# Optimization experiments

Hardware: AMD Instinct MI355X
Metric: run time of the kernel (lower is better)

The kernel has to match this reference:

```python
import jax, jax.numpy as jnp
import numpy as np

DS = 4  # pooling / upsample factor


def _avg_pool(t, ds):
    B, C, H, W = t.shape
    return t.reshape(B, C, H // ds, ds, W // ds, ds).mean(axis=(3, 5))


def setup_inputs() -> dict:
    key = jax.random.key(0)
    ks = jax.random.split(key, 8)
    B, C, H, W = 8, 512, 128, 128
    Ck = C // 4
    inp = jax.random.normal(ks[0], (B, C, H, W), dtype=jnp.float32)
    c2 = jax.random.normal(ks[1], (B, C, H, W), dtype=jnp.float32)
    # 1x1 conv weights == dense matrices over channel dim (with bias, as nn.Conv2d default)
    Wq = jax.random.normal(ks[2], (Ck, C), dtype=jnp.float32) * 0.02
    bq = jax.random.normal(ks[3], (Ck,), dtype=jnp.float32) * 0.02
    Wk = jax.random.normal(ks[4], (Ck, C), dtype=jnp.float32) * 0.02
    bk = jax.random.normal(ks[5], (Ck,), dtype=jnp.float32) * 0.02
    Wv = jax.random.normal(ks[6], (C, C), dtype=jnp.float32) * 0.02
    bv = jax.random.normal(ks[7], (C,), dtype=jnp.float32) * 0.02
    return {"input": inp, "c2": c2, "Wq": Wq, "bq": bq, "Wk": Wk, "bk": bk, "Wv": Wv, "bv": bv}


def reference(input, c2, Wq, bq, Wk, bk, Wv, bv):
    # Note: the torch module's `gamma` parameter is NOT used in forward; faithful omission.
    x = _avg_pool(input, DS)  # [B,C,h,w]
    y = _avg_pool(c2, DS)
    B, C, h, w = x.shape
    N = h * w
    Ck = Wq.shape[0]
    xf = x.reshape(B, C, N)
    yf = y.reshape(B, C, N)
    q = jnp.einsum('oc,bcn->bon', Wq, xf) + bq[None, :, None]  # [B,Ck,N]
    k = jnp.einsum('oc,bcn->bon', Wk, yf) + bk[None, :, None]  # [B,Ck,N]
    v = jnp.einsum('oc,bcn->bon', Wv, yf) + bv[None, :, None]  # [B,C,N]
    scale = jnp.asarray(Ck, x.dtype) ** -0.5
    energy = jnp.einsum('bon,bom->bnm', q, k) * scale  # [B,N,N] = q^T k
    attn = jax.nn.softmax(energy, axis=-1)
    out = jnp.einsum('bcm,bnm->bcn', v, attn)  # v @ attn^T
    out = out.reshape(B, C, h, w)
    # F.interpolate with default mode='nearest' and size = exact integer multiple -> repeat
    out = jnp.repeat(jnp.repeat(out, DS, axis=2), DS, axis=3)
    return out + c2
```

## Files before the change

### kernel.cpp

```cpp
#include <hip/hip_runtime.h>
#include <stdint.h>
#include <stddef.h>

#define Bn   8
#define Cn   512
#define CKn  128
#define Hn   128
#define Nn   1024

typedef float f32x4 __attribute__((ext_vector_type(4)));
typedef short bf16x8 __attribute__((ext_vector_type(8)));

__device__ __forceinline__ uint16_t f2b(float f) {
  uint32_t x = __float_as_uint(f);
  uint32_t r = (x + 0x7FFFu + ((x >> 16) & 1u)) >> 16;
  return (uint16_t)r;
}

__device__ __forceinline__ void gld_lds16(const uint16_t* g, short* lds_base, int lane) {
#if __has_builtin(__builtin_amdgcn_global_load_lds)
  __builtin_amdgcn_global_load_lds(
      (const __attribute__((address_space(1))) void*)g,
      (__attribute__((address_space(3))) void*)lds_base, 16, 0, 0);
#else
  *(bf16x8*)(lds_base + lane * 8) = *(const bf16x8*)g;
#endif
}

__device__ __forceinline__ void gemm128(const uint16_t* __restrict__ A,
                                        const uint16_t* __restrict__ Bt,
                                        int lda, int ldb, int K,
                                        short* As, short* Bs, f32x4 acc[4][4]) {
  const int tid  = threadIdx.x;
  const int lane = tid & 63;
  const int wave = tid >> 6;
  const int quad = lane >> 4, l16 = lane & 15;
  const int rin  = lane >> 2, cc = lane & 3;
  const int wr = wave >> 1, wc = wave & 1;
  for (int kt = 0; kt < K; kt += 32) {
    __syncthreads();
    gld_lds16(A  + (size_t)(wave * 32 +      rin) * lda + kt + cc * 8, As + wave * 1024,       lane);
    gld_lds16(A  + (size_t)(wave * 32 + 16 + rin) * lda + kt + cc * 8, As + wave * 1024 + 512, lane);
    gld_lds16(Bt + (size_t)(wave * 32 +      rin) * ldb + kt + cc * 8, Bs + wave * 1024,       lane);
    gld_lds16(Bt + (size_t)(wave * 32 + 16 + rin) * ldb + kt + cc * 8, Bs + wave * 1024 + 512, lane);
    __syncthreads();
    bf16x8 af[4], bfr[4];
#pragma unroll
    for (int i = 0; i < 4; ++i)
      af[i] = *(const bf16x8*)(As + (wr * 64 + i * 16 + l16) * 32 + quad * 8);
#pragma unroll
    for (int j = 0; j < 4; ++j)
      bfr[j] = *(const bf16x8*)(Bs + (wc * 64 + j * 16 + l16) * 32 + quad * 8);
#pragma unroll
    for (int i = 0; i < 4; ++i)
#pragma unroll
      for (int j = 0; j < 4; ++j)
        acc[i][j] = __builtin_amdgcn_mfma_f32_16x16x32_bf16(af[i], bfr[j], acc[i][j], 0, 0, 0);
  }
}

#define EPI_VARS \
  const int lane = threadIdx.x & 63; const int wave = threadIdx.x >> 6; \
  const int quad = lane >> 4, l16 = lane & 15; \
  const int wr = wave >> 1, wc = wave & 1;

__global__ __launch_bounds__(256) void wconv_kernel(
    const float* __restrict__ Wq, const float* __restrict__ Wk, const float* __restrict__ Wv,
    uint16_t* __restrict__ Wqb, uint16_t* __restrict__ Wkb, uint16_t* __restrict__ Wvb) {
  int i = blockIdx.x * 256 + threadIdx.x;
  if (i < CKn * Cn) { Wqb[i] = f2b(Wq[i]); Wkb[i] = f2b(Wk[i]); }
  Wvb[i] = f2b(Wv[i]);
}

__global__ __launch_bounds__(1024) void pool_kernel(
    const float* __restrict__ input, const float* __restrict__ c2,
    uint16_t* __restrict__ xT, uint16_t* __restrict__ yT) {
  const int cblk = blockIdx.x, ph = blockIdx.y;
  const int b = blockIdx.z >> 1, src = blockIdx.z & 1;
  const float* in = src ? c2 : input;
  uint16_t* out = src ? yT : xT;
  const int tw = threadIdx.x & 31, tc = threadIdx.x >> 5;
  const int c = cblk * 32 + tc;
  const float* p = in + (((size_t)(b * Cn + c) * Hn) + ph * 4) * Hn + tw * 4;
  float s = 0.f;
#pragma unroll
  for (int r = 0; r < 4; ++r) {
    float4 t = *(const float4*)(p + (size_t)r * Hn);
    s += t.x + t.y + t.z + t.w;
  }
  __shared__ float tile[32][33];
  tile[tw][tc] = s * 0.0625f;
  __syncthreads();
  const int tn = threadIdx.x >> 5, tcc = threadIdx.x & 31;
  out[((size_t)b * Nn + ph * 32 + tn) * Cn + cblk * 32 + tcc] = f2b(tile[tn][tcc]);
}

__global__ __launch_bounds__(256) void qkv_kernel(
    const uint16_t* __restrict__ Wqb, const uint16_t* __restrict__ Wkb, const uint16_t* __restrict__ Wvb,
    const float* __restrict__ bq, const float* __restrict__ bk, const float* __restrict__ bv,
    const uint16_t* __restrict__ xT, const uint16_t* __restrict__ yT,
    uint16_t* __restrict__ qT, uint16_t* __restrict__ kT, uint16_t* __restrict__ vm) {
  __shared__ short As[4096], Bs[4096];
  const int b = blockIdx.y;
  const int r = blockIdx.x;
  const int mt = r >> 3, nt = r & 7;
  int op, m0; const uint16_t* A; const float* bias;
  if (mt == 0)      { op = 0; m0 = 0;              A = Wqb;                     bias = bq; }
  else if (mt == 1) { op = 1; m0 = 0;              A = Wkb;                     bias = bk; }
  else              { op = 2; m0 = (mt - 2) * 128; A = Wvb + (size_t)m0 * Cn;   bias = bv; }
  const uint16_t* Bt = ((op == 0) ? xT : yT) + (size_t)b * Nn * Cn + (size_t)nt * 128 * Cn;
  f32x4 acc[4][4];
#pragma unroll
  for (int i = 0; i < 4; ++i)
#pragma unroll
    for (int j = 0; j < 4; ++j) acc[i][j] = (f32x4)0.f;
  gemm128(A, Bt, Cn, Cn, Cn, As, Bs, acc);
  EPI_VARS;
#pragma unroll
  for (int i = 0; i < 4; ++i)
#pragma unroll
    for (int j = 0; j < 4; ++j)
#pragma unroll
      for (int rg = 0; rg < 4; ++rg) {
        int m = m0 + wr * 64 + i * 16 + quad * 4 + rg;
        int n = nt * 128 + wc * 64 + j * 16 + l16;
        float val = acc[i][j][rg] + bias[m];
        if (op == 2) vm[(size_t)(b * Cn + m) * Nn + n] = f2b(val);
        else {
          uint16_t* dst = (op == 0) ? qT : kT;
          dst[(size_t)(b * Nn + n) * CKn + m] = f2b(val);
        }
      }
}

__global__ __launch_bounds__(1024) void esm_kernel(
    const uint16_t* __restrict__ qT, const uint16_t* __restrict__ kT,
    uint16_t* __restrict__ attn) {
  const int b = blockIdx.y, n0 = blockIdx.x * 16;
  const int tid = threadIdx.x, lane = tid & 63, w = tid >> 6;
  const int quad = lane >> 4, l16 = lane & 15;
  const uint16_t* qb = qT + (size_t)(b * Nn + n0) * CKn;
  const uint16_t* kb = kT + (size_t)(b * Nn + w * 64) * CKn;
  f32x4 acc[4];
#pragma unroll
  for (int j = 0; j < 4; ++j) acc[j] = (f32x4)0.f;
#pragma unroll
  for (int kt = 0; kt < CKn; kt += 32) {
    bf16x8 af = *(const bf16x8*)(qb + (size_t)l16 * CKn + kt + quad * 8);
    bf16x8 bfr[4];
#pragma unroll
    for (int j = 0; j < 4; ++j)
      bfr[j] = *(const bf16x8*)(kb + (size_t)(j * 16 + l16) * CKn + kt + quad * 8);
#pragma unroll
    for (int j = 0; j < 4; ++j)
      acc[j] = __builtin_amdgcn_mfma_f32_16x16x32_bf16(af, bfr[j], acc[j], 0, 0, 0);
  }
  const float scale = 0.08838834764831845f;
#pragma unroll
  for (int j = 0; j < 4; ++j) acc[j] *= scale;

  __shared__ float red[16][16];
  __shared__ float gout[16];
  float mx[4];
#pragma unroll
  for (int rg = 0; rg < 4; ++rg) {
    mx[rg] = fmaxf(fmaxf(acc[0][rg], acc[1][rg]), fmaxf(acc[2][rg], acc[3][rg]));
#pragma unroll
    for (int off = 1; off < 16; off <<= 1) mx[rg] = fmaxf(mx[rg], __shfl_xor(mx[rg], off, 64));
  }
  if (l16 == 0) {
#pragma unroll
    for (int rg = 0; rg < 4; ++rg) red[quad * 4 + rg][w] = mx[rg];
  }
  __syncthreads();
  if (tid < 16) {
    float g = -3.4e38f;
#pragma unroll
    for (int ww = 0; ww < 16; ++ww) g = fmaxf(g, red[tid][ww]);
    gout[tid] = g;
  }
  __syncthreads();
  float rmax[4];
#pragma unroll
  for (int rg = 0; rg < 4; ++rg) rmax[rg] = gout[quad * 4 + rg];
  float sm[4] = {0.f, 0.f, 0.f, 0.f};
#pragma unroll
  for (int j = 0; j < 4; ++j)
#pragma unroll
    for (int rg = 0; rg < 4; ++rg) {
      float p = __expf(acc[j][rg] - rmax[rg]);
      acc[j][rg] = p;
      sm[rg] += p;
    }
#pragma unroll
  for (int rg = 0; rg < 4; ++rg)
#pragma unroll
    for (int off = 1; off < 16; off <<= 1) sm[rg] += __shfl_xor(sm[rg], off, 64);
  if (l16 == 0) {
#pragma unroll
    for (int rg = 0; rg < 4; ++rg) red[quad * 4 + rg][w] = sm[rg];
  }
  __syncthreads();
  if (tid < 16) {
    float s = 0.f;
#pragma unroll
    for (int ww = 0; ww < 16; ++ww) s += red[tid][ww];
    gout[tid] = 1.f / s;
  }
  __syncthreads();
#pragma unroll
  for (int rg = 0; rg < 4; ++rg) {
    float inv = gout[quad * 4 + rg];
    uint16_t* arow = attn + (size_t)(b * Nn + n0 + quad * 4 + rg) * Nn + w * 64;
#pragma unroll
    for (int j = 0; j < 4; ++j) arow[j * 16 + l16] = f2b(acc[j][rg] * inv);
  }
}

__global__ __launch_bounds__(256) void outup_kernel(
    const uint16_t* __restrict__ vm, const uint16_t* __restrict__ attn,
    const float* __restrict__ c2, float* __restrict__ out) {
  __shared__ short As[4096], Bs[4096];
  const int b = blockIdx.y;
  const int r = blockIdx.x, mt = r >> 3, nt = r & 7;
  const uint16_t* A  = vm   + (size_t)b * Cn * Nn + (size_t)mt * 128 * Nn;
  const uint16_t* Bt = attn + (size_t)b * Nn * Nn + (size_t)nt * 128 * Nn;
  f32x4 acc[4][4];
#pragma unroll
  for (int i = 0; i < 4; ++i)
#pragma unroll
    for (int j = 0; j < 4; ++j) acc[i][j] = (f32x4)0.f;
  gemm128(A, Bt, Nn, Nn, Nn, As, Bs, acc);
  EPI_VARS;
#pragma unroll
  for (int i = 0; i < 4; ++i)
#pragma unroll
    for (int j = 0; j < 4; ++j) {
      const int n  = nt * 128 + wc * 64 + j * 16 + l16;
      const int ph = n >> 5, pw = n & 31;
#pragma unroll
      for (int rg = 0; rg < 4; ++rg) {
        const int c = mt * 128 + wr * 64 + i * 16 + quad * 4 + rg;
        const float v = acc[i][j][rg];
        const size_t base = (((size_t)(b * Cn + c) * Hn) + ph * 4) * Hn + pw * 4;
#pragma unroll
        for (int rr = 0; rr < 4; ++rr) {
          float4 t4 = *(const float4*)(c2 + base + (size_t)rr * Hn);
          t4.x += v; t4.y += v; t4.z += v; t4.w += v;
          *(float4*)(out + base + (size_t)rr * Hn) = t4;
        }
      }
    }
}

extern "C" void kernel_launch(void* const* d_in, const int* in_sizes, int n_in,
                              void* d_out, int out_size, void* d_ws, size_t ws_size,
                              hipStream_t stream) {
  const float* input = (const float*)d_in[0];
  const float* c2    = (const float*)d_in[1];
  const float* Wq    = (const float*)d_in[2];
  const float* bq    = (const float*)d_in[3];
  const float* Wk    = (const float*)d_in[4];
  const float* bk    = (const float*)d_in[5];
  const float* Wv    = (const float*)d_in[6];
  const float* bv    = (const float*)d_in[7];
  float* out = (float*)d_out;
  uint8_t* ws = (uint8_t*)d_ws;

  uint16_t* xT   = (uint16_t*)(ws + 0);
  uint16_t* yT   = (uint16_t*)(ws + 8388608);
  uint16_t* Wqb  = (uint16_t*)(ws + 16777216);
  uint16_t* Wkb  = (uint16_t*)(ws + 16908288);
  uint16_t* Wvb  = (uint16_t*)(ws + 17039360);
  uint16_t* qT   = (uint16_t*)(ws + 17563648);
  uint16_t* kT   = (uint16_t*)(ws + 19660800);
  uint16_t* vm   = (uint16_t*)(ws + 21757952);
  uint16_t* attn = (uint16_t*)(ws + 30146560);

  hipLaunchKernelGGL(wconv_kernel, dim3(1024), dim3(256), 0, stream,
                     Wq, Wk, Wv, Wqb, Wkb, Wvb);
  hipLaunchKernelGGL(pool_kernel, dim3(16, 32, 16), dim3(1024), 0, stream,
                     input, c2, xT, yT);
  hipLaunchKernelGGL(qkv_kernel, dim3(48, 8), dim3(256), 0, stream,
                     Wqb, Wkb, Wvb, bq, bk, bv, xT, yT, qT, kT, vm);
  hipLaunchKernelGGL(esm_kernel, dim3(64, 8), dim3(1024), 0, stream, qT, kT, attn);
  hipLaunchKernelGGL(outup_kernel, dim3(32, 8), dim3(256), 0, stream,
                     vm, attn, c2, out);
}
```

Measured before the change: 722.9 us.

## Split output GEMM from upsample-add and use 64x128 tiles

```diff
diff --git a/kernel.cpp b/kernel.cpp
--- a/kernel.cpp
+++ b/kernel.cpp
@@ -59,6 +59,30 @@
   }
 }
 
+__device__ __forceinline__ void gemm64x128(const uint16_t* __restrict__ A,
+                                           const uint16_t* __restrict__ Bt,
+                                           int lda, int ldb, int K,
+                                           short* As, short* Bs, f32x4 acc[8]) {
+  const int tid  = threadIdx.x;
+  const int lane = tid & 63;
+  const int wave = tid >> 6;
+  const int quad = lane >> 4, l16 = lane & 15;
+  const int rin  = lane >> 2, cc = lane & 3;
+  for (int kt = 0; kt < K; kt += 32) {
+    __syncthreads();
+    gld_lds16(A + (size_t)(wave * 16 + rin) * lda + kt + cc * 8, As + wave * 512, lane);
+    gld_lds16(Bt + (size_t)(wave * 32 + rin) * ldb + kt + cc * 8, Bs + wave * 1024, lane);
+    gld_lds16(Bt + (size_t)(wave * 32 + 16 + rin) * ldb + kt + cc * 8, Bs + wave * 1024 + 512, lane);
+    __syncthreads();
+    bf16x8 af = *(const bf16x8*)(As + (wave * 16 + l16) * 32 + quad * 8);
+#pragma unroll
+    for (int j = 0; j < 8; ++j) {
+      bf16x8 bfr = *(const bf16x8*)(Bs + (j * 16 + l16) * 32 + quad * 8);
+      acc[j] = __builtin_amdgcn_mfma_f32_16x16x32_bf16(af, bfr, acc[j], 0, 0, 0);
+    }
+  }
+}
+
 #define EPI_VARS \
   const int lane = threadIdx.x & 63; const int wave = threadIdx.x >> 6; \
   const int quad = lane >> 4, l16 = lane & 15; \
@@ -217,40 +241,43 @@
   }
 }
 
-__global__ __launch_bounds__(256) void outup_kernel(
+__global__ __launch_bounds__(256) void outg_kernel(
     const uint16_t* __restrict__ vm, const uint16_t* __restrict__ attn,
-    const float* __restrict__ c2, float* __restrict__ out) {
-  __shared__ short As[4096], Bs[4096];
-  const int b = blockIdx.y;
-  const int r = blockIdx.x, mt = r >> 3, nt = r & 7;
-  const uint16_t* A  = vm   + (size_t)b * Cn * Nn + (size_t)mt * 128 * Nn;
+    float* __restrict__ osm) {
+  __shared__ short As[2048], Bs[4096];
+  const int bx = blockIdx.x;
+  const int b = bx >> 6, r = bx & 63, mt = r >> 3, nt = r & 7;
+  const uint16_t* A  = vm   + (size_t)b * Cn * Nn + (size_t)mt * 64 * Nn;
   const uint16_t* Bt = attn + (size_t)b * Nn * Nn + (size_t)nt * 128 * Nn;
-  f32x4 acc[4][4];
-#pragma unroll
-  for (int i = 0; i < 4; ++i)
-#pragma unroll
-    for (int j = 0; j < 4; ++j) acc[i][j] = (f32x4)0.f;
-  gemm128(A, Bt, Nn, Nn, Nn, As, Bs, acc);
+  f32x4 acc[8];
+#pragma unroll
+  for (int j = 0; j < 8; ++j) acc[j] = (f32x4)0.f;
+  gemm64x128(A, Bt, Nn, Nn, Nn, As, Bs, acc);
   EPI_VARS;
-#pragma unroll
-  for (int i = 0; i < 4; ++i)
-#pragma unroll
-    for (int j = 0; j < 4; ++j) {
-      const int n  = nt * 128 + wc * 64 + j * 16 + l16;
-      const int ph = n >> 5, pw = n & 31;
-#pragma unroll
-      for (int rg = 0; rg < 4; ++rg) {
-        const int c = mt * 128 + wr * 64 + i * 16 + quad * 4 + rg;
-        const float v = acc[i][j][rg];
-        const size_t base = (((size_t)(b * Cn + c) * Hn) + ph * 4) * Hn + pw * 4;
-#pragma unroll
-        for (int rr = 0; rr < 4; ++rr) {
-          float4 t4 = *(const float4*)(c2 + base + (size_t)rr * Hn);
-          t4.x += v; t4.y += v; t4.z += v; t4.w += v;
-          *(float4*)(out + base + (size_t)rr * Hn) = t4;
-        }
-      }
+  (void)wr; (void)wc;
+#pragma unroll
+  for (int j = 0; j < 8; ++j)
+#pragma unroll
+    for (int rg = 0; rg < 4; ++rg) {
+      int c = mt * 64 + wave * 16 + quad * 4 + rg;
+      int n = nt * 128 + j * 16 + l16;
+      osm[(size_t)b * Cn * Nn + (size_t)c * Nn + n] = acc[j][rg];
     }
+}
+
+__global__ __launch_bounds__(256) void upsample_kernel(
+    const float* __restrict__ osm, const float* __restrict__ c2,
+    float* __restrict__ out) {
+  const int t = blockIdx.x * 256 + threadIdx.x;
+  const int ww4 = t & 31;
+  const int hh  = (t >> 5) & 127;
+  const int cb  = t >> 12;
+  const int n = (hh >> 2) * 32 + ww4;
+  const float val = osm[((size_t)cb << 10) + n];
+  const size_t base = (((size_t)cb * Hn) + hh) * Hn + ww4 * 4;
+  float4 t4 = *(const float4*)(c2 + base);
+  t4.x += val; t4.y += val; t4.z += val; t4.w += val;
+  *(float4*)(out + base) = t4;
 }
 
 extern "C" void kernel_launch(void* const* d_in, const int* in_sizes, int n_in,
@@ -276,6 +303,7 @@
   uint16_t* kT   = (uint16_t*)(ws + 19660800);
   uint16_t* vm   = (uint16_t*)(ws + 21757952);
   uint16_t* attn = (uint16_t*)(ws + 30146560);
+  float*    osm  = (float*)   (ws + 46923776);
 
   hipLaunchKernelGGL(wconv_kernel, dim3(1024), dim3(256), 0, stream,
                      Wq, Wk, Wv, Wqb, Wkb, Wvb);
@@ -284,6 +312,6 @@
   hipLaunchKernelGGL(qkv_kernel, dim3(48, 8), dim3(256), 0, stream,
                      Wqb, Wkb, Wvb, bq, bk, bv, xT, yT, qT, kT, vm);
   hipLaunchKernelGGL(esm_kernel, dim3(64, 8), dim3(1024), 0, stream, qT, kT, attn);
-  hipLaunchKernelGGL(outup_kernel, dim3(32, 8), dim3(256), 0, stream,
-                     vm, attn, c2, out);
-}
+  hipLaunchKernelGGL(outg_kernel, dim3(512), dim3(256), 0, stream, vm, attn, osm);
+  hipLaunchKernelGGL(upsample_kernel, dim3(65536), dim3(256), 0, stream, osm, c2, out);
+}
```

After: 711.5 us. About the same (-1.6%).
